# Performance work log

Hardware: AMD Instinct MI355X
Metric: run time of the kernel (lower is better)

## Reference

```python
import jax, jax.numpy as jnp
import numpy as np

SOLVER_STEPS = 10
POINT_DIM = 2
CONTEXT_DIM = 128
HIDDEN_DIM = 256


def setup_inputs() -> dict:
    key = jax.random.key(0)
    ks = jax.random.split(key, 8)
    B, N = 64, 4096
    in_dim = POINT_DIM + 1 + CONTEXT_DIM  # 131
    std = 0.1  # torch nn.init.normal_(std=0.1)
    x = jax.random.normal(ks[0], (B, N, POINT_DIM), jnp.float32)
    context = jax.random.normal(ks[1], (B, CONTEXT_DIM), jnp.float32)
    w1 = std * jax.random.normal(ks[2], (in_dim, HIDDEN_DIM), jnp.float32)
    w2 = std * jax.random.normal(ks[3], (HIDDEN_DIM, HIDDEN_DIM), jnp.float32)
    w3 = std * jax.random.normal(ks[4], (HIDDEN_DIM, HIDDEN_DIM), jnp.float32)
    w4 = std * 0.1 * jax.random.normal(ks[5], (HIDDEN_DIM, POINT_DIM), jnp.float32)  # last layer weight * 0.1
    b1 = jnp.zeros((HIDDEN_DIM,), jnp.float32)
    b2 = jnp.zeros((HIDDEN_DIM,), jnp.float32)
    b3 = jnp.zeros((HIDDEN_DIM,), jnp.float32)
    b4 = jnp.zeros((POINT_DIM,), jnp.float32)
    return {"x": x, "context": context, "w1": w1, "b1": b1, "w2": w2, "b2": b2,
            "w3": w3, "b3": b3, "w4": w4, "b4": b4}


def _mlp(pts, t, ctx, w1, b1, w2, b2, w3, b3, w4, b4):
    # pts: [B,N,2], ctx: [B,N,C] -> velocity [B,N,2]
    B, N, _ = pts.shape
    t_vec = jnp.full((B, N, 1), t, dtype=pts.dtype)
    h = jnp.concatenate([pts, t_vec, ctx], axis=-1)
    h = jax.nn.silu(h @ w1 + b1)  # Swish == silu
    h = jax.nn.silu(h @ w2 + b2)
    h = jax.nn.silu(h @ w3 + b3)
    return h @ w4 + b4


def reference(x, context, w1, b1, w2, b2, w3, b3, w4, b4):
    B, N, D = x.shape
    ctx = jnp.broadcast_to(context[:, None, :], (B, N, context.shape[-1]))
    dt = jnp.asarray(1.0 / SOLVER_STEPS, x.dtype)
    ts = jnp.linspace(0.0, 1.0, SOLVER_STEPS + 1, dtype=x.dtype)[:SOLVER_STEPS]
    e0 = jnp.broadcast_to(jnp.array([1.0, 0.0], x.dtype), x.shape)
    e1 = jnp.broadcast_to(jnp.array([0.0, 1.0], x.dtype), x.shape)

    def step(carry, t_i):
        pts, log_det = carry
        f = lambda p: _mlp(p, t_i, ctx, w1, b1, w2, b2, w3, b3, w4, b4)
        # exact divergence = trace of per-point 2x2 Jacobian via two JVPs
        v, j0 = jax.jvp(f, (pts,), (e0,))
        _, j1 = jax.jvp(f, (pts,), (e1,))
        div = (j0[..., 0] + j1[..., 1])[..., None]  # [B,N,1]
        return (pts + v * dt, log_det + div * dt), None

    init = (x, jnp.zeros((B, N, 1), x.dtype))
    (final_pts, log_det), _ = jax.lax.scan(step, init, ts)
    final_log_det = log_det[..., 0].sum(axis=1, keepdims=True)  # [B,1]
    return final_pts, final_log_det
```

## Files before the change

kernel.cpp:

```cpp
#include <hip/hip_runtime.h>

typedef short bf16x8 __attribute__((ext_vector_type(8)));
typedef float f32x4 __attribute__((ext_vector_type(4)));

#define AS 264
#define T0OFF (32 * AS)
#define T1OFF (64 * AS)

__device__ __forceinline__ unsigned short f2bf(float f) {
    union { float f; unsigned int u; } v; v.f = f;
    unsigned int u = v.u + 0x7FFFu + ((v.u >> 16) & 1u);
    return (unsigned short)(u >> 16);
}
__device__ __forceinline__ unsigned cvtpk(float a, float b) {
    unsigned r;
    asm("v_cvt_pk_bf16_f32 %0, %1, %2" : "=v"(r) : "v"(a), "v"(b));
    return r;
}
__device__ __forceinline__ float bf2f(unsigned int h) {
    union { unsigned int u; float f; } v; v.u = h << 16; return v.f;
}
__device__ __forceinline__ float sigm(float x) {
    return __builtin_amdgcn_rcpf(1.0f + __expf(-x));
}

struct f4s { float v[4]; };
__device__ __forceinline__ f4s ld4(const float* p) {
    float4 t = *(const float4*)p;
    f4s r; r.v[0] = t.x; r.v[1] = t.y; r.v[2] = t.z; r.v[3] = t.w; return r;
}


__global__ void k_base(const float* __restrict__ ctx,
                       const float* __restrict__ w1,
                       const float* __restrict__ b1,
                       float* __restrict__ base) {
    const int b = blockIdx.x, n = threadIdx.x;
    float acc = b1[n];
    for (int c = 0; c < 128; ++c)
        acc += ctx[b * 128 + c] * w1[(3 + c) * 256 + n];
    base[b * 256 + n] = acc;
}

__global__ void k_frag(const float* __restrict__ w,
                       unsigned short* __restrict__ wf) {
    const int t = blockIdx.x * blockDim.x + threadIdx.x;
    const int j = t & 7, n = (t >> 3) & 255, q = (t >> 11) & 3, kk = t >> 13;
    wf[t] = f2bf(w[(kk * 32 + q * 8 + j) * 256 + n]);
}

#define MFMA3(frag_base, buf)                                                              \
    {                                                                                      \
        const bf16x8 fP  = *(const bf16x8*)(Asl + (frag_base));                            \
        const bf16x8 fT0 = *(const bf16x8*)(Asl + (frag_base) + T0OFF);                    \
        const bf16x8 fT1 = *(const bf16x8*)(Asl + (frag_base) + T1OFF);                    \
        _Pragma("unroll")                                                                  \
        for (int nb = 0; nb < 4; ++nb) {                                                   \
            aP[nb]  = __builtin_amdgcn_mfma_f32_16x16x32_bf16(buf[nb], fP,  aP[nb],  0, 0, 0); \
            aT0[nb] = __builtin_amdgcn_mfma_f32_16x16x32_bf16(buf[nb], fT0, aT0[nb], 0, 0, 0); \
            aT1[nb] = __builtin_amdgcn_mfma_f32_16x16x32_bf16(buf[nb], fT1, aT1[nb], 0, 0, 0); \
        }                                                                                  \
    }

__device__ __forceinline__ void do_gemm_direct(const unsigned short* __restrict__ wf,
                                               const unsigned short* Asl,
                                               int raP, int base0,
                                               f32x4 aP[4], f32x4 aT0[4], f32x4 aT1[4]) {
    const bf16x8* __restrict__ wp = (const bf16x8*)wf;
    bf16x8 bufA[4], bufB[4];
#pragma unroll
    for (int nb = 0; nb < 4; ++nb) bufA[nb] = wp[base0 + nb * 16];
#pragma unroll 1
    for (int kk = 0; kk < 8; kk += 2) {
#pragma unroll
        for (int nb = 0; nb < 4; ++nb) bufB[nb] = wp[(kk + 1) * 1024 + base0 + nb * 16];
        MFMA3(raP + kk * 32, bufA);
        if (kk + 2 < 8) {
#pragma unroll
            for (int nb = 0; nb < 4; ++nb) bufA[nb] = wp[(kk + 2) * 1024 + base0 + nb * 16];
        }
        MFMA3(raP + (kk + 1) * 32, bufB);
    }
}

__device__ __forceinline__ void el_write(unsigned short* Asl,
                                         const f32x4* aP, const f32x4* aT0, const f32x4* aT1,
                                         int ebase) {
#pragma unroll
    for (int nb = 0; nb < 4; ++nb) {
        float h[4], t0[4], t1[4];
#pragma unroll
        for (int e = 0; e < 4; ++e) {
            const float pre = aP[nb][e];
            const float s = sigm(pre);
            const float hv = pre * s;
            const float dd = fmaf(hv, 1.0f - s, s);
            h[e]  = hv;
            t0[e] = dd * aT0[nb][e];
            t1[e] = dd * aT1[nb][e];
        }
        uint2 v0, v1, v2;
        v0.x = cvtpk(h[0],  h[1]);  v0.y = cvtpk(h[2],  h[3]);
        v1.x = cvtpk(t0[0], t0[1]); v1.y = cvtpk(t0[2], t0[3]);
        v2.x = cvtpk(t1[0], t1[1]); v2.y = cvtpk(t1[2], t1[3]);
        *(uint2*)(Asl + ebase + nb * 16)         = v0;
        *(uint2*)(Asl + ebase + nb * 16 + T0OFF) = v1;
        *(uint2*)(Asl + ebase + nb * 16 + T1OFF) = v2;
    }
}

__launch_bounds__(512, 4)
__global__ void k_main(const float* __restrict__ x,
                       const float* __restrict__ w1,
                       const float* __restrict__ b2g,
                       const float* __restrict__ b3g,
                       const float* __restrict__ w4g,
                       const float* __restrict__ b4g,
                       const unsigned short* __restrict__ w2f,
                       const unsigned short* __restrict__ w3f,
                       const float* __restrict__ basep,
                       float* __restrict__ ldacc,
                       float* __restrict__ out) {
    __shared__ unsigned short Asl[96 * AS];
    __shared__ float w1r[3][256];
    __shared__ float basel[256];
    __shared__ float w40[256], w41[256];
    __shared__ float b2l[256], b3l[256];
    __shared__ float px[32][2];
    __shared__ float pld[32];

    const int tid = threadIdx.x;
    const int wg = blockIdx.x;
    const int b = wg >> 7;
    const int n0 = (wg & 127) << 5;

    for (int i = tid; i < 768; i += 512) w1r[i >> 8][i & 255] = w1[i];
    if (tid < 256) {
        basel[tid] = basep[b * 256 + tid];
        w40[tid] = w4g[2 * tid]; w41[tid] = w4g[2 * tid + 1];
        b2l[tid] = b2g[tid];     b3l[tid] = b3g[tid];
    }
    if (tid < 64) ((float*)px)[tid] = x[((b << 12) + n0) * 2 + tid];
    if (tid < 32) pld[tid] = 0.0f;

    const int lane = tid & 63, wave = tid >> 6;
    const int m = lane & 15, q = lane >> 4;
    const int tw = wave & 1;
    const int nbb = (wave >> 1) << 2;
    const int raPq  = (tw * 16 + m) * AS + q * 8;
    const int ebase = (tw * 16 + m) * AS + nbb * 16 + (q << 2);
    const int base0 = q * 256 + nbb * 16 + m;
    const int bbase = nbb * 16 + (q << 2);

    const int p4 = tid >> 4;
    const int ic = tid & 15;

    const float b40 = b4g[0], b41 = b4g[1];
    __syncthreads();

#pragma unroll 1
    for (int st = 0; st < 10; ++st) {
        const float ti = 0.1f * (float)st;
        const float x0 = px[p4][0];
        const float x1 = px[p4][1];
#pragma unroll
        for (int g = 0; g < 4; ++g) {
            const int cb = g * 64 + (ic << 2);
            const f4s wa = ld4(&w1r[0][cb]);
            const f4s wb = ld4(&w1r[1][cb]);
            const f4s wc = ld4(&w1r[2][cb]);
            const f4s bs = ld4(&basel[cb]);
            float hf[4], t0f[4], t1f[4];
#pragma unroll
            for (int e = 0; e < 4; ++e) {
                const float pre = x0 * wa.v[e] + x1 * wb.v[e] + ti * wc.v[e] + bs.v[e];
                const float s = sigm(pre);
                const float h = pre * s;
                const float d = fmaf(h, 1.0f - s, s);
                hf[e]  = h;
                t0f[e] = d * wa.v[e];
                t1f[e] = d * wb.v[e];
            }
            uint2 v0, v1, v2;
            v0.x = cvtpk(hf[0],  hf[1]);  v0.y = cvtpk(hf[2],  hf[3]);
            v1.x = cvtpk(t0f[0], t0f[1]); v1.y = cvtpk(t0f[2], t0f[3]);
            v2.x = cvtpk(t1f[0], t1f[1]); v2.y = cvtpk(t1f[2], t1f[3]);
            *(uint2*)(Asl + p4 * AS + cb) = v0;
            *(uint2*)(Asl + T0OFF + p4 * AS + cb) = v1;
            *(uint2*)(Asl + T1OFF + p4 * AS + cb) = v2;
        }
        __syncthreads();

        f32x4 aP[4], aT0[4], aT1[4];
#pragma unroll
        for (int i = 0; i < 4; ++i) {
            const float4 bv = *(const float4*)&b2l[bbase + i * 16];
            aP[i]  = f32x4{bv.x, bv.y, bv.z, bv.w};
            aT0[i] = f32x4{0.f, 0.f, 0.f, 0.f};
            aT1[i] = f32x4{0.f, 0.f, 0.f, 0.f};
        }
        do_gemm_direct(w2f, Asl, raPq, base0, aP, aT0, aT1);
        __syncthreads();
        el_write(Asl, aP, aT0, aT1, ebase);
        __syncthreads();

#pragma unroll
        for (int i = 0; i < 4; ++i) {
            const float4 bv = *(const float4*)&b3l[bbase + i * 16];
            aP[i]  = f32x4{bv.x, bv.y, bv.z, bv.w};
            aT0[i] = f32x4{0.f, 0.f, 0.f, 0.f};
            aT1[i] = f32x4{0.f, 0.f, 0.f, 0.f};
        }
        do_gemm_direct(w3f, Asl, raPq, base0, aP, aT0, aT1);
        __syncthreads();
        el_write(Asl, aP, aT0, aT1, ebase);
        __syncthreads();

        {
            float v0 = 0.f, v1 = 0.f, j00 = 0.f, j11 = 0.f;
#pragma unroll
            for (int g = 0; g < 4; ++g) {
                const int cb = g * 64 + (ic << 2);
                const uint2 hv  = *(const uint2*)(Asl + p4 * AS + cb);
                const uint2 t0v = *(const uint2*)(Asl + T0OFF + p4 * AS + cb);
                const uint2 t1v = *(const uint2*)(Asl + T1OFF + p4 * AS + cb);
                const f4s wa = ld4(&w40[cb]);
                const f4s wb = ld4(&w41[cb]);
                const unsigned hu[4]  = { hv.x & 0xffffu,  hv.x >> 16,  hv.y & 0xffffu,  hv.y >> 16 };
                const unsigned t0u[4] = { t0v.x & 0xffffu, t0v.x >> 16, t0v.y & 0xffffu, t0v.y >> 16 };
                const unsigned t1u[4] = { t1v.x & 0xffffu, t1v.x >> 16, t1v.y & 0xffffu, t1v.y >> 16 };
#pragma unroll
                for (int e = 0; e < 4; ++e) {
                    const float h = bf2f(hu[e]);
                    v0  += h * wa.v[e];
                    v1  += h * wb.v[e];
                    j00 += bf2f(t0u[e]) * wa.v[e];
                    j11 += bf2f(t1u[e]) * wb.v[e];
                }
            }
#pragma unroll
            for (int o = 1; o < 16; o <<= 1) {
                v0  += __shfl_xor(v0, o);
                v1  += __shfl_xor(v1, o);
                j00 += __shfl_xor(j00, o);
                j11 += __shfl_xor(j11, o);
            }
            if (ic == 0) {
                px[p4][0] += 0.1f * (v0 + b40);
                px[p4][1] += 0.1f * (v1 + b41);
                pld[p4]   += 0.1f * (j00 + j11);
            }
        }
    }

    if (ic == 0) {
        out[((b << 12) + n0 + p4) * 2]     = px[p4][0];
        out[((b << 12) + n0 + p4) * 2 + 1] = px[p4][1];
    }
    __syncthreads();
    if (wave == 0) {
        float v = (lane < 32) ? pld[lane] : 0.0f;
#pragma unroll
        for (int o = 32; o > 0; o >>= 1) v += __shfl_xor(v, o);
        if (lane == 0) atomicAdd(ldacc + b, v);
    }
}

__global__ void k_fin(const float* __restrict__ ldacc, float* __restrict__ out) {
    out[524288 + threadIdx.x] = ldacc[threadIdx.x];
}

extern "C" void kernel_launch(void* const* d_in, const int* in_sizes, int n_in,
                              void* d_out, int out_size, void* d_ws, size_t ws_size,
                              hipStream_t stream) {
    const float* x   = (const float*)d_in[0];
    const float* ctx = (const float*)d_in[1];
    const float* w1  = (const float*)d_in[2];
    const float* b1  = (const float*)d_in[3];
    const float* w2  = (const float*)d_in[4];
    const float* b2  = (const float*)d_in[5];
    const float* w3  = (const float*)d_in[6];
    const float* b3  = (const float*)d_in[7];
    const float* w4  = (const float*)d_in[8];
    const float* b4  = (const float*)d_in[9];

    char* ws = (char*)d_ws;
    unsigned short* w2f = (unsigned short*)ws;
    unsigned short* w3f = (unsigned short*)(ws + 131072);
    float* basep = (float*)(ws + 262144);
    float* ldacc = (float*)(ws + 327680);
    float* out = (float*)d_out;

    hipMemsetAsync(ldacc, 0, 64 * sizeof(float), stream);
    k_base<<<dim3(64), dim3(256), 0, stream>>>(ctx, w1, b1, basep);
    k_frag<<<dim3(128), dim3(512), 0, stream>>>(w2, w2f);
    k_frag<<<dim3(128), dim3(512), 0, stream>>>(w3, w3f);
    k_main<<<dim3(8192), dim3(512), 0, stream>>>(x, w1, b2, b3, w4, b4, w2f, w3f, basep, ldacc, out);
    k_fin<<<dim3(1), dim3(64), 0, stream>>>(ldacc, out);
}
```

Baseline: 2.268 ms.

## Switch hidden GEMMs to 32x32x16 MFMA with per-wave 32-column tiles

```diff
diff --git a/kernel.cpp b/kernel.cpp
--- a/kernel.cpp
+++ b/kernel.cpp
@@ -2,6 +2,7 @@
 
 typedef short bf16x8 __attribute__((ext_vector_type(8)));
 typedef float f32x4 __attribute__((ext_vector_type(4)));
+typedef float f32x16 __attribute__((ext_vector_type(16)));
 
 #define AS 264
 #define T0OFF (32 * AS)
@@ -45,67 +46,69 @@
 __global__ void k_frag(const float* __restrict__ w,
                        unsigned short* __restrict__ wf) {
     const int t = blockIdx.x * blockDim.x + threadIdx.x;
-    const int j = t & 7, n = (t >> 3) & 255, q = (t >> 11) & 3, kk = t >> 13;
-    wf[t] = f2bf(w[(kk * 32 + q * 8 + j) * 256 + n]);
-}
-
-#define MFMA3(frag_base, buf)                                                              \
-    {                                                                                      \
-        const bf16x8 fP  = *(const bf16x8*)(Asl + (frag_base));                            \
-        const bf16x8 fT0 = *(const bf16x8*)(Asl + (frag_base) + T0OFF);                    \
-        const bf16x8 fT1 = *(const bf16x8*)(Asl + (frag_base) + T1OFF);                    \
-        _Pragma("unroll")                                                                  \
-        for (int nb = 0; nb < 4; ++nb) {                                                   \
-            aP[nb]  = __builtin_amdgcn_mfma_f32_16x16x32_bf16(buf[nb], fP,  aP[nb],  0, 0, 0); \
-            aT0[nb] = __builtin_amdgcn_mfma_f32_16x16x32_bf16(buf[nb], fT0, aT0[nb], 0, 0, 0); \
-            aT1[nb] = __builtin_amdgcn_mfma_f32_16x16x32_bf16(buf[nb], fT1, aT1[nb], 0, 0, 0); \
-        }                                                                                  \
-    }
-
-__device__ __forceinline__ void do_gemm_direct(const unsigned short* __restrict__ wf,
-                                               const unsigned short* Asl,
-                                               int raP, int base0,
-                                               f32x4 aP[4], f32x4 aT0[4], f32x4 aT1[4]) {
+    const int j = t & 7, lane = (t >> 3) & 63, hb = (t >> 9) & 7, kk = t >> 12;
+    const int c = kk * 16 + (lane >> 5) * 8 + j;
+    const int h = hb * 32 + (lane & 31);
+    wf[t] = f2bf(w[c * 256 + h]);
+}
+
+__device__ __forceinline__ void do_gemm32(const unsigned short* __restrict__ wf,
+                                          const unsigned short* Asl,
+                                          int abase, int wub,
+                                          f32x16& aP, f32x16& aT0, f32x16& aT1) {
     const bf16x8* __restrict__ wp = (const bf16x8*)wf;
-    bf16x8 bufA[4], bufB[4];
-#pragma unroll
-    for (int nb = 0; nb < 4; ++nb) bufA[nb] = wp[base0 + nb * 16];
+    bf16x8 buf[4];
+#pragma unroll
+    for (int i = 0; i < 4; ++i) buf[i] = wp[wub + i * 512];
 #pragma unroll 1
-    for (int kk = 0; kk < 8; kk += 2) {
-#pragma unroll
-        for (int nb = 0; nb < 4; ++nb) bufB[nb] = wp[(kk + 1) * 1024 + base0 + nb * 16];
-        MFMA3(raP + kk * 32, bufA);
-        if (kk + 2 < 8) {
-#pragma unroll
-            for (int nb = 0; nb < 4; ++nb) bufA[nb] = wp[(kk + 2) * 1024 + base0 + nb * 16];
-        }
-        MFMA3(raP + (kk + 1) * 32, bufB);
-    }
-}
-
-__device__ __forceinline__ void el_write(unsigned short* Asl,
-                                         const f32x4* aP, const f32x4* aT0, const f32x4* aT1,
-                                         int ebase) {
-#pragma unroll
-    for (int nb = 0; nb < 4; ++nb) {
+    for (int kk = 0; kk < 12; kk += 4) {
+#pragma unroll
+        for (int u = 0; u < 4; ++u) {
+            const int koff = (kk + u) * 16;
+            const bf16x8 fP  = *(const bf16x8*)(Asl + abase + koff);
+            const bf16x8 fT0 = *(const bf16x8*)(Asl + abase + koff + T0OFF);
+            const bf16x8 fT1 = *(const bf16x8*)(Asl + abase + koff + T1OFF);
+            aP  = __builtin_amdgcn_mfma_f32_32x32x16_bf16(buf[u], fP,  aP,  0, 0, 0);
+            aT0 = __builtin_amdgcn_mfma_f32_32x32x16_bf16(buf[u], fT0, aT0, 0, 0, 0);
+            aT1 = __builtin_amdgcn_mfma_f32_32x32x16_bf16(buf[u], fT1, aT1, 0, 0, 0);
+            buf[u] = wp[wub + (kk + 4 + u) * 512];
+        }
+    }
+#pragma unroll
+    for (int u = 0; u < 4; ++u) {
+        const int koff = (12 + u) * 16;
+        const bf16x8 fP  = *(const bf16x8*)(Asl + abase + koff);
+        const bf16x8 fT0 = *(const bf16x8*)(Asl + abase + koff + T0OFF);
+        const bf16x8 fT1 = *(const bf16x8*)(Asl + abase + koff + T1OFF);
+        aP  = __builtin_amdgcn_mfma_f32_32x32x16_bf16(buf[u], fP,  aP,  0, 0, 0);
+        aT0 = __builtin_amdgcn_mfma_f32_32x32x16_bf16(buf[u], fT0, aT0, 0, 0, 0);
+        aT1 = __builtin_amdgcn_mfma_f32_32x32x16_bf16(buf[u], fT1, aT1, 0, 0, 0);
+    }
+}
+
+__device__ __forceinline__ void el_write32(unsigned short* Asl,
+                                           const f32x16& aP, const f32x16& aT0, const f32x16& aT1,
+                                           int ebase) {
+#pragma unroll
+    for (int g = 0; g < 4; ++g) {
         float h[4], t0[4], t1[4];
 #pragma unroll
         for (int e = 0; e < 4; ++e) {
-            const float pre = aP[nb][e];
+            const float pre = aP[4 * g + e];
             const float s = sigm(pre);
             const float hv = pre * s;
             const float dd = fmaf(hv, 1.0f - s, s);
             h[e]  = hv;
-            t0[e] = dd * aT0[nb][e];
-            t1[e] = dd * aT1[nb][e];
+            t0[e] = dd * aT0[4 * g + e];
+            t1[e] = dd * aT1[4 * g + e];
         }
         uint2 v0, v1, v2;
         v0.x = cvtpk(h[0],  h[1]);  v0.y = cvtpk(h[2],  h[3]);
         v1.x = cvtpk(t0[0], t0[1]); v1.y = cvtpk(t0[2], t0[3]);
         v2.x = cvtpk(t1[0], t1[1]); v2.y = cvtpk(t1[2], t1[3]);
-        *(uint2*)(Asl + ebase + nb * 16)         = v0;
-        *(uint2*)(Asl + ebase + nb * 16 + T0OFF) = v1;
-        *(uint2*)(Asl + ebase + nb * 16 + T1OFF) = v2;
+        *(uint2*)(Asl + ebase + 8 * g)         = v0;
+        *(uint2*)(Asl + ebase + 8 * g + T0OFF) = v1;
+        *(uint2*)(Asl + ebase + 8 * g + T1OFF) = v2;
     }
 }
 
@@ -144,13 +147,12 @@
     if (tid < 32) pld[tid] = 0.0f;
 
     const int lane = tid & 63, wave = tid >> 6;
-    const int m = lane & 15, q = lane >> 4;
-    const int tw = wave & 1;
-    const int nbb = (wave >> 1) << 2;
-    const int raPq  = (tw * 16 + m) * AS + q * 8;
-    const int ebase = (tw * 16 + m) * AS + nbb * 16 + (q << 2);
-    const int base0 = q * 256 + nbb * 16 + m;
-    const int bbase = nbb * 16 + (q << 2);
+    const int p = lane & 31, kh = lane >> 5;
+    const int hb = wave;
+    const int abase = p * AS + kh * 8;
+    const int ebase = p * AS + hb * 32 + kh * 4;
+    const int wub   = hb * 64 + lane;
+    const int bbase = hb * 32 + kh * 4;
 
     const int p4 = tid >> 4;
     const int ic = tid & 15;
@@ -191,29 +193,31 @@
         }
         __syncthreads();
 
-        f32x4 aP[4], aT0[4], aT1[4];
-#pragma unroll
-        for (int i = 0; i < 4; ++i) {
-            const float4 bv = *(const float4*)&b2l[bbase + i * 16];
-            aP[i]  = f32x4{bv.x, bv.y, bv.z, bv.w};
-            aT0[i] = f32x4{0.f, 0.f, 0.f, 0.f};
-            aT1[i] = f32x4{0.f, 0.f, 0.f, 0.f};
-        }
-        do_gemm_direct(w2f, Asl, raPq, base0, aP, aT0, aT1);
-        __syncthreads();
-        el_write(Asl, aP, aT0, aT1, ebase);
-        __syncthreads();
-
-#pragma unroll
-        for (int i = 0; i < 4; ++i) {
-            const float4 bv = *(const float4*)&b3l[bbase + i * 16];
-            aP[i]  = f32x4{bv.x, bv.y, bv.z, bv.w};
-            aT0[i] = f32x4{0.f, 0.f, 0.f, 0.f};
-            aT1[i] = f32x4{0.f, 0.f, 0.f, 0.f};
-        }
-        do_gemm_direct(w3f, Asl, raPq, base0, aP, aT0, aT1);
-        __syncthreads();
-        el_write(Asl, aP, aT0, aT1, ebase);
+        f32x16 aP, aT0, aT1;
+#pragma unroll
+        for (int g = 0; g < 4; ++g) {
+            const float4 bv = *(const float4*)&b2l[bbase + 8 * g];
+            aP[4 * g + 0] = bv.x; aP[4 * g + 1] = bv.y;
+            aP[4 * g + 2] = bv.z; aP[4 * g + 3] = bv.w;
+        }
+#pragma unroll
+        for (int r = 0; r < 16; ++r) { aT0[r] = 0.f; aT1[r] = 0.f; }
+        do_gemm32(w2f, Asl, abase, wub, aP, aT0, aT1);
+        __syncthreads();
+        el_write32(Asl, aP, aT0, aT1, ebase);
+        __syncthreads();
+
+#pragma unroll
+        for (int g = 0; g < 4; ++g) {
+            const float4 bv = *(const float4*)&b3l[bbase + 8 * g];
+            aP[4 * g + 0] = bv.x; aP[4 * g + 1] = bv.y;
+            aP[4 * g + 2] = bv.z; aP[4 * g + 3] = bv.w;
+        }
+#pragma unroll
+        for (int r = 0; r < 16; ++r) { aT0[r] = 0.f; aT1[r] = 0.f; }
+        do_gemm32(w3f, Asl, abase, wub, aP, aT0, aT1);
+        __syncthreads();
+        el_write32(Asl, aP, aT0, aT1, ebase);
         __syncthreads();
 
         {
```

After: 2.401 ms. 1.06x slower.

## Shrink blocks to 16 points and fuse layer-3 SiLU with output projection

Applied to the files above, without the earlier changes.

```diff
diff --git a/kernel.cpp b/kernel.cpp
--- a/kernel.cpp
+++ b/kernel.cpp
@@ -4,8 +4,8 @@
 typedef float f32x4 __attribute__((ext_vector_type(4)));
 
 #define AS 264
-#define T0OFF (32 * AS)
-#define T1OFF (64 * AS)
+#define T0OFF (16 * AS)
+#define T1OFF (32 * AS)
 
 __device__ __forceinline__ unsigned short f2bf(float f) {
     union { float f; unsigned int u; } v; v.f = f;
@@ -16,9 +16,6 @@
     unsigned r;
     asm("v_cvt_pk_bf16_f32 %0, %1, %2" : "=v"(r) : "v"(a), "v"(b));
     return r;
-}
-__device__ __forceinline__ float bf2f(unsigned int h) {
-    union { unsigned int u; float f; } v; v.u = h << 16; return v.f;
 }
 __device__ __forceinline__ float sigm(float x) {
     return __builtin_amdgcn_rcpf(1.0f + __expf(-x));
@@ -49,7 +46,7 @@
     wf[t] = f2bf(w[(kk * 32 + q * 8 + j) * 256 + n]);
 }
 
-#define MFMA3(frag_base, buf)                                                              \
+#define MFMA12(frag_base, buf)                                                             \
     {                                                                                      \
         const bf16x8 fP  = *(const bf16x8*)(Asl + (frag_base));                            \
         const bf16x8 fT0 = *(const bf16x8*)(Asl + (frag_base) + T0OFF);                    \
@@ -74,12 +71,12 @@
     for (int kk = 0; kk < 8; kk += 2) {
 #pragma unroll
         for (int nb = 0; nb < 4; ++nb) bufB[nb] = wp[(kk + 1) * 1024 + base0 + nb * 16];
-        MFMA3(raP + kk * 32, bufA);
+        MFMA12(raP + kk * 32, bufA);
         if (kk + 2 < 8) {
 #pragma unroll
             for (int nb = 0; nb < 4; ++nb) bufA[nb] = wp[(kk + 2) * 1024 + base0 + nb * 16];
         }
-        MFMA3(raP + (kk + 1) * 32, bufB);
+        MFMA12(raP + (kk + 1) * 32, bufB);
     }
 }
 
@@ -109,7 +106,7 @@
     }
 }
 
-__launch_bounds__(512, 4)
+__launch_bounds__(256, 4)
 __global__ void k_main(const float* __restrict__ x,
                        const float* __restrict__ w1,
                        const float* __restrict__ b2g,
@@ -121,41 +118,39 @@
                        const float* __restrict__ basep,
                        float* __restrict__ ldacc,
                        float* __restrict__ out) {
-    __shared__ unsigned short Asl[96 * AS];
+    __shared__ unsigned short Asl[48 * AS];
     __shared__ float w1r[3][256];
     __shared__ float basel[256];
-    __shared__ float w40[256], w41[256];
     __shared__ float b2l[256], b3l[256];
-    __shared__ float px[32][2];
-    __shared__ float pld[32];
+    __shared__ float w40l[256], w41l[256];
+    __shared__ float px[16][2];
+    __shared__ float pslab[4][16][4];
 
     const int tid = threadIdx.x;
     const int wg = blockIdx.x;
-    const int b = wg >> 7;
-    const int n0 = (wg & 127) << 5;
-
-    for (int i = tid; i < 768; i += 512) w1r[i >> 8][i & 255] = w1[i];
-    if (tid < 256) {
-        basel[tid] = basep[b * 256 + tid];
-        w40[tid] = w4g[2 * tid]; w41[tid] = w4g[2 * tid + 1];
-        b2l[tid] = b2g[tid];     b3l[tid] = b3g[tid];
-    }
-    if (tid < 64) ((float*)px)[tid] = x[((b << 12) + n0) * 2 + tid];
-    if (tid < 32) pld[tid] = 0.0f;
+    const int b = wg >> 8;
+    const int n0 = (wg & 255) << 4;
+
+    for (int i = tid; i < 768; i += 256) w1r[i >> 8][i & 255] = w1[i];
+    basel[tid] = basep[b * 256 + tid];
+    b2l[tid]  = b2g[tid];
+    b3l[tid]  = b3g[tid];
+    w40l[tid] = w4g[2 * tid];
+    w41l[tid] = w4g[2 * tid + 1];
+    if (tid < 32) ((float*)px)[tid] = x[((b << 12) + n0) * 2 + tid];
 
     const int lane = tid & 63, wave = tid >> 6;
     const int m = lane & 15, q = lane >> 4;
-    const int tw = wave & 1;
-    const int nbb = (wave >> 1) << 2;
-    const int raPq  = (tw * 16 + m) * AS + q * 8;
-    const int ebase = (tw * 16 + m) * AS + nbb * 16 + (q << 2);
-    const int base0 = q * 256 + nbb * 16 + m;
-    const int bbase = nbb * 16 + (q << 2);
+    const int raPq  = m * AS + q * 8;
+    const int ebase = m * AS + wave * 64 + (q << 2);
+    const int base0 = q * 256 + wave * 64 + m;
+    const int bbase = wave * 64 + (q << 2);
 
     const int p4 = tid >> 4;
     const int ic = tid & 15;
 
     const float b40 = b4g[0], b41 = b4g[1];
+    float pldreg = 0.0f;
     __syncthreads();
 
 #pragma unroll 1
@@ -212,57 +207,57 @@
             aT1[i] = f32x4{0.f, 0.f, 0.f, 0.f};
         }
         do_gemm_direct(w3f, Asl, raPq, base0, aP, aT0, aT1);
-        __syncthreads();
-        el_write(Asl, aP, aT0, aT1, ebase);
-        __syncthreads();
 
         {
-            float v0 = 0.f, v1 = 0.f, j00 = 0.f, j11 = 0.f;
-#pragma unroll
-            for (int g = 0; g < 4; ++g) {
-                const int cb = g * 64 + (ic << 2);
-                const uint2 hv  = *(const uint2*)(Asl + p4 * AS + cb);
-                const uint2 t0v = *(const uint2*)(Asl + T0OFF + p4 * AS + cb);
-                const uint2 t1v = *(const uint2*)(Asl + T1OFF + p4 * AS + cb);
-                const f4s wa = ld4(&w40[cb]);
-                const f4s wb = ld4(&w41[cb]);
-                const unsigned hu[4]  = { hv.x & 0xffffu,  hv.x >> 16,  hv.y & 0xffffu,  hv.y >> 16 };
-                const unsigned t0u[4] = { t0v.x & 0xffffu, t0v.x >> 16, t0v.y & 0xffffu, t0v.y >> 16 };
-                const unsigned t1u[4] = { t1v.x & 0xffffu, t1v.x >> 16, t1v.y & 0xffffu, t1v.y >> 16 };
+            float v0p = 0.f, v1p = 0.f, j00p = 0.f, j11p = 0.f;
+#pragma unroll
+            for (int nb = 0; nb < 4; ++nb) {
+                const f4s wA = ld4(&w40l[bbase + nb * 16]);
+                const f4s wB = ld4(&w41l[bbase + nb * 16]);
 #pragma unroll
                 for (int e = 0; e < 4; ++e) {
-                    const float h = bf2f(hu[e]);
-                    v0  += h * wa.v[e];
-                    v1  += h * wb.v[e];
-                    j00 += bf2f(t0u[e]) * wa.v[e];
-                    j11 += bf2f(t1u[e]) * wb.v[e];
+                    const float pre = aP[nb][e];
+                    const float s = sigm(pre);
+                    const float hv = pre * s;
+                    const float dd = fmaf(hv, 1.0f - s, s);
+                    v0p  = fmaf(hv, wA.v[e], v0p);
+                    v1p  = fmaf(hv, wB.v[e], v1p);
+                    j00p = fmaf(dd * aT0[nb][e], wA.v[e], j00p);
+                    j11p = fmaf(dd * aT1[nb][e], wB.v[e], j11p);
                 }
             }
-#pragma unroll
-            for (int o = 1; o < 16; o <<= 1) {
-                v0  += __shfl_xor(v0, o);
-                v1  += __shfl_xor(v1, o);
-                j00 += __shfl_xor(j00, o);
-                j11 += __shfl_xor(j11, o);
+            v0p  += __shfl_xor(v0p, 16);  v0p  += __shfl_xor(v0p, 32);
+            v1p  += __shfl_xor(v1p, 16);  v1p  += __shfl_xor(v1p, 32);
+            j00p += __shfl_xor(j00p, 16); j00p += __shfl_xor(j00p, 32);
+            j11p += __shfl_xor(j11p, 16); j11p += __shfl_xor(j11p, 32);
+            if (lane < 16) {
+                float4 t; t.x = v0p; t.y = v1p; t.z = j00p; t.w = j11p;
+                *(float4*)&pslab[wave][m][0] = t;
             }
-            if (ic == 0) {
-                px[p4][0] += 0.1f * (v0 + b40);
-                px[p4][1] += 0.1f * (v1 + b41);
-                pld[p4]   += 0.1f * (j00 + j11);
-            }
-        }
-    }
-
-    if (ic == 0) {
-        out[((b << 12) + n0 + p4) * 2]     = px[p4][0];
-        out[((b << 12) + n0 + p4) * 2 + 1] = px[p4][1];
-    }
-    __syncthreads();
-    if (wave == 0) {
-        float v = (lane < 32) ? pld[lane] : 0.0f;
-#pragma unroll
-        for (int o = 32; o > 0; o >>= 1) v += __shfl_xor(v, o);
-        if (lane == 0) atomicAdd(ldacc + b, v);
+        }
+        __syncthreads();
+
+        if (tid < 16) {
+            const float4 a0 = *(const float4*)&pslab[0][tid][0];
+            const float4 a1 = *(const float4*)&pslab[1][tid][0];
+            const float4 a2 = *(const float4*)&pslab[2][tid][0];
+            const float4 a3 = *(const float4*)&pslab[3][tid][0];
+            const float v0 = a0.x + a1.x + a2.x + a3.x;
+            const float v1 = a0.y + a1.y + a2.y + a3.y;
+            const float dv = (a0.z + a1.z + a2.z + a3.z) + (a0.w + a1.w + a2.w + a3.w);
+            px[tid][0] += 0.1f * (v0 + b40);
+            px[tid][1] += 0.1f * (v1 + b41);
+            pldreg     += 0.1f * dv;
+        }
+        __syncthreads();
+    }
+
+    if (tid < 16) {
+        float2 o; o.x = px[tid][0]; o.y = px[tid][1];
+        *(float2*)&out[((b << 12) + n0 + tid) * 2] = o;
+#pragma unroll
+        for (int o2 = 8; o2 > 0; o2 >>= 1) pldreg += __shfl_xor(pldreg, o2);
+        if (tid == 0) atomicAdd(ldacc + b, pldreg);
     }
 }
 
@@ -295,6 +290,6 @@
     k_base<<<dim3(64), dim3(256), 0, stream>>>(ctx, w1, b1, basep);
     k_frag<<<dim3(128), dim3(512), 0, stream>>>(w2, w2f);
     k_frag<<<dim3(128), dim3(512), 0, stream>>>(w3, w3f);
-    k_main<<<dim3(8192), dim3(512), 0, stream>>>(x, w1, b2, b3, w4, b4, w2f, w3f, basep, ldacc, out);
+    k_main<<<dim3(16384), dim3(256), 0, stream>>>(x, w1, b2, b3, w4, b4, w2f, w3f, basep, ldacc, out);
     k_fin<<<dim3(1), dim3(64), 0, stream>>>(ldacc, out);
 }
```

Result: faster. 2.189 ms (-3.5%).
